# Optimization experiments

Hardware: AMD Instinct MI355X
Metric: run time of the kernel (lower is better)

The kernel has to match this reference:

```python
import jax, jax.numpy as jnp
import numpy as np

N_EMBD = 768
NUM_HEADS = 12
NEG_INF = -1e38


def setup_inputs() -> dict:
    key = jax.random.key(0)
    kx, kq, kk, kv, ko, kb = jax.random.split(key, 6)
    B, S, E = 2, 2048, N_EMBD
    scale = 1.0 / np.sqrt(E)
    return {
        "x": jax.random.normal(kx, (B, S, E), dtype=jnp.float32),
        "Wq": jax.random.normal(kq, (E, E), dtype=jnp.float32) * scale,
        "Wk": jax.random.normal(kk, (E, E), dtype=jnp.float32) * scale,
        "Wv": jax.random.normal(kv, (E, E), dtype=jnp.float32) * scale,
        "Wo": jax.random.normal(ko, (E, E), dtype=jnp.float32) * scale,
        "bo": jax.random.normal(kb, (E,), dtype=jnp.float32) * 0.01,
    }


def reference(x, Wq, Wk, Wv, Wo, bo):
    B, S, E = x.shape
    H = NUM_HEADS
    D = E // H

    def split_heads(t):  # [B,S,E] -> [B,H,S,D]
        return t.reshape(B, S, H, D).transpose(0, 2, 1, 3)

    # torch Linear (no bias): y = x @ W.T
    q = split_heads(jnp.einsum('bse,fe->bsf', x, Wq))
    k = split_heads(jnp.einsum('bse,fe->bsf', x, Wk))
    v = split_heads(jnp.einsum('bse,fe->bsf', x, Wv))

    # NOTE: original module does NOT scale by 1/sqrt(head_dim) — faithful.
    scores = jnp.einsum('bhqd,bhkd->bhqk', q, k)  # [B,H,S,S]
    causal_mask = (1.0 - jnp.tril(jnp.ones((S, S), dtype=x.dtype))) * NEG_INF
    probs = jax.nn.softmax(scores + causal_mask, axis=-1)
    attn = jnp.einsum('bhqk,bhkd->bhqd', probs, v)  # [B,H,S,D]

    merged = attn.transpose(0, 2, 1, 3).reshape(B, S, E)
    out = jnp.einsum('bse,fe->bsf', merged, Wo) + bo
    return (out, k, v)
```

## Files before the change

### kernel.cpp

```cpp
#include <hip/hip_runtime.h>
#include <hip/hip_bf16.h>

#define S_LEN 2048
#define EMB 768
#define NH 12
#define HD 64
#define L2E 1.44269504088896340736f

typedef __attribute__((ext_vector_type(8))) short short8;
typedef __attribute__((ext_vector_type(4))) float f32x4;

typedef __attribute__((address_space(3))) void lds_t;
typedef __attribute__((address_space(1))) const void gbl_t;

__device__ __forceinline__ void gload16(const void* g, void* l) {
  __builtin_amdgcn_global_load_lds((gbl_t*)g, (lds_t*)l, 16, 0, 0);
}

__device__ __forceinline__ short f2bf(float f) {
  union { float f; unsigned u; } v; v.f = f;
  unsigned r = v.u + 0x7FFFu + ((v.u >> 16) & 1u);
  return (short)(r >> 16);
}

__device__ __forceinline__ unsigned pkbf(float a, float b) {
  unsigned r;
  asm("v_cvt_pk_bf16_f32 %0, %1, %2" : "=v"(r) : "v"(a), "v"(b));
  return r;
}

__global__ void cvt_all(const float* __restrict__ x,
                        const float* __restrict__ Wq, const float* __restrict__ Wk,
                        const float* __restrict__ Wv, const float* __restrict__ Wo,
                        short* __restrict__ xb, short* __restrict__ Wb,
                        short* __restrict__ Wob) {
  int bid = blockIdx.x, tid = threadIdx.x;
  const float* src;
  short* dst;
  int off;
  if (bid < 3072) {
    src = x; dst = xb; off = bid * 1024 + tid * 4;
  } else {
    int wb = bid - 3072;
    int sec = wb / 576;
    off = (wb % 576) * 1024 + tid * 4;
    src = sec == 0 ? Wq : sec == 1 ? Wk : sec == 2 ? Wv : Wo;
    dst = sec < 3 ? Wb + sec * 589824 : Wob;
  }
  float4 v = *reinterpret_cast<const float4*>(src + off);
  short4 o;
  o.x = f2bf(v.x); o.y = f2bf(v.y); o.z = f2bf(v.z); o.w = f2bf(v.w);
  *reinterpret_cast<short4*>(dst + off) = o;
}

template<int MODE>
__global__ __launch_bounds__(256)
void gemm_nt(const short* __restrict__ A, const short* __restrict__ B,
             float* __restrict__ outk, float* __restrict__ outv,
             short* __restrict__ qb, short* __restrict__ kb, short* __restrict__ vtb,
             float* __restrict__ outp, const float* __restrict__ bias) {
  const int K = EMB;
  const int NT = K / 64;
  __shared__ __align__(16) char RAW[128 * 132 * 4];
  short (*As)[128][64] = (short(*)[128][64])RAW;
  short (*Bs)[128][64] = (short(*)[128][64])(RAW + 32768);
  float (*Cl)[132] = (float(*)[132])RAW;
  int tid = threadIdx.x;
  int lane = tid & 63, wid = tid >> 6;
  int wm = wid >> 1, wn = wid & 1;
  int r16 = lane & 15, g4 = lane >> 4;
  int m0 = blockIdx.y * 128, n0 = blockIdx.x * 128;
  int lrow = lane >> 3, lchunk = lane & 7;
  int lcolsw = ((lchunk ^ lrow) * 8);
  f32x4 acc[4][4] = {};

#define STAGEG(BUF, K0) do {                                          \
    _Pragma("unroll")                                                 \
    for (int i = 0; i < 4; i++) {                                     \
      int r = wid * 32 + i * 8 + lrow;                                \
      gload16(A + (long)(m0 + r) * K + (K0) + lcolsw, &As[BUF][r][lchunk * 8]); \
      gload16(B + (long)(n0 + r) * K + (K0) + lcolsw, &Bs[BUF][r][lchunk * 8]); \
    } } while (0)

  STAGEG(0, 0);
  int cur = 0;
  for (int t = 0; t < NT; t++) {
    if (t + 1 < NT) {
      STAGEG(cur ^ 1, (t + 1) * 64);
      asm volatile("s_waitcnt vmcnt(8)" ::: "memory");
    } else {
      asm volatile("s_waitcnt vmcnt(0)" ::: "memory");
    }
    __builtin_amdgcn_sched_barrier(0);
    __builtin_amdgcn_s_barrier();
    __builtin_amdgcn_sched_barrier(0);
#pragma unroll
    for (int s = 0; s < 2; s++) {
      int csw = ((s * 4 + g4) ^ (r16 & 7)) * 8;
      short8 af[4], bf[4];
#pragma unroll
      for (int tt = 0; tt < 4; tt++) {
        af[tt] = *reinterpret_cast<const short8*>(&As[cur][wm * 64 + tt * 16 + r16][csw]);
        bf[tt] = *reinterpret_cast<const short8*>(&Bs[cur][wn * 64 + tt * 16 + r16][csw]);
      }
#pragma unroll
      for (int mt = 0; mt < 4; mt++)
#pragma unroll
        for (int nt = 0; nt < 4; nt++)
          acc[mt][nt] = __builtin_amdgcn_mfma_f32_16x16x32_bf16(af[mt], bf[nt], acc[mt][nt], 0, 0, 0);
    }
    __builtin_amdgcn_sched_barrier(0);
    __builtin_amdgcn_s_barrier();
    cur ^= 1;
  }
#undef STAGEG

  if (MODE == 1) {
#pragma unroll
    for (int mt = 0; mt < 4; mt++) {
      int nbase = m0 + wm * 64 + mt * 16 + g4 * 4;
#pragma unroll
      for (int nt = 0; nt < 4; nt++) {
        int f = n0 + wn * 64 + nt * 16 + r16;
#pragma unroll
        for (int r = 0; r < 4; r++)
          outp[(long)(nbase + r) * EMB + f] = acc[mt][nt][r] + bias[f];
      }
    }
    return;
  }

  const int bx = blockIdx.x;
  const int sec = bx / 6;
  const int h0 = (bx % 6) * 2;
  const int b = m0 >> 11, s0l = m0 & 2047;

  if (sec == 2) {
#pragma unroll
    for (int mt = 0; mt < 4; mt++) {
      int sg = s0l + wm * 64 + mt * 16 + g4 * 4;
#pragma unroll
      for (int nt = 0; nt < 4; nt++) {
        int fl = wn * 64 + nt * 16 + r16;
        int h = h0 + (fl >> 6), d = fl & 63;
        int bh = b * NH + h;
        short4 o;
        o.x = f2bf(acc[mt][nt][0]); o.y = f2bf(acc[mt][nt][1]);
        o.z = f2bf(acc[mt][nt][2]); o.w = f2bf(acc[mt][nt][3]);
        *reinterpret_cast<short4*>(
            &vtb[((long)(bh * 32 + (sg >> 6)) * 64 + d) * 64 + (sg & 63)]) = o;
      }
    }
  }

#pragma unroll
  for (int mt = 0; mt < 4; mt++) {
    int rl = wm * 64 + mt * 16 + g4 * 4;
#pragma unroll
    for (int nt = 0; nt < 4; nt++) {
      int fl = wn * 64 + nt * 16 + r16;
#pragma unroll
      for (int r = 0; r < 4; r++) Cl[rl + r][fl] = acc[mt][nt][r];
    }
  }
  __syncthreads();

  {
    int row = tid >> 1, cb = (tid & 1) * 32;
#pragma unroll
    for (int hh = 0; hh < 2; hh++) {
      const float* src = &Cl[row][hh * 64 + cb];
      long base = ((long)(b * NH + h0 + hh) * S_LEN + s0l) * HD + (long)row * 64 + cb;
      if (sec == 0) {
        short* dq = qb + base;
#pragma unroll
        for (int c = 0; c < 4; c++) {
          f32x4 a = *reinterpret_cast<const f32x4*>(src + c * 8);
          f32x4 bb = *reinterpret_cast<const f32x4*>(src + c * 8 + 4);
          short8 o;
#pragma unroll
          for (int j = 0; j < 4; j++) { o[j] = f2bf(a[j]); o[4 + j] = f2bf(bb[j]); }
          *reinterpret_cast<short8*>(dq + c * 8) = o;
        }
      } else if (sec == 1) {
        float* dk = outk + base;
        short* dkb = kb + base;
#pragma unroll
        for (int c = 0; c < 4; c++) {
          f32x4 a = *reinterpret_cast<const f32x4*>(src + c * 8);
          f32x4 bb = *reinterpret_cast<const f32x4*>(src + c * 8 + 4);
          *reinterpret_cast<f32x4*>(dk + c * 8) = a;
          *reinterpret_cast<f32x4*>(dk + c * 8 + 4) = bb;
          short8 o;
#pragma unroll
          for (int j = 0; j < 4; j++) { o[j] = f2bf(a[j]); o[4 + j] = f2bf(bb[j]); }
          *reinterpret_cast<short8*>(dkb + c * 8) = o;
        }
      } else {
        float* dv = outv + base;
#pragma unroll
        for (int c = 0; c < 8; c++)
          *reinterpret_cast<f32x4*>(dv + c * 4) =
              *reinterpret_cast<const f32x4*>(src + c * 4);
      }
    }
  }
}

__global__ __launch_bounds__(256)
void flash_attn15(const short* __restrict__ qb, const short* __restrict__ kb,
                  const short* __restrict__ vtb, short* __restrict__ mb) {
  const int tid = threadIdx.x;
  const int w = tid >> 6, lane = tid & 63;
  const int r16 = lane & 15, g4 = lane >> 4;
  const int id = blockIdx.x;
  const int xcd = id & 7, u = id >> 3;
  const int bh = xcd + 8 * (u % 3);
  const int qt = 31 - u / 3;
  const int q0 = qt * 64 + w * 16;
  const int nkt = qt + 1;

  const short* qh = qb + (long)bh * S_LEN * HD;
  const short* kh = kb + (long)bh * S_LEN * HD;
  const short* vh = vtb + (long)bh * S_LEN * HD;

  __shared__ __align__(16) short KVl[2][2][64][64];
  __shared__ __align__(16) short Pa[4][16][40];
  __shared__ __align__(16) short Pb[4][16][40];
  __shared__ __align__(16) float sca_lds[4][16];
  float* Olds = (float*)&KVl[0][0][0][0];

  const int srow = tid >> 3, schunk = tid & 7;
  const short* ksrc = kh + srow * HD + ((schunk ^ (srow & 7)) * 8);
  const short* vsrc = vh + srow * 64 + ((schunk ^ (srow & 7)) * 8);
#define STAGE(BUF, KT) do {                                          \
    long _off = (long)(KT) * 4096;                                   \
    gload16(ksrc + _off,           &KVl[BUF][0][srow][schunk * 8]);      \
    gload16(ksrc + _off + 32 * HD, &KVl[BUF][0][srow + 32][schunk * 8]); \
    gload16(vsrc + _off,           &KVl[BUF][1][srow][schunk * 8]);      \
    gload16(vsrc + _off + 32 * 64, &KVl[BUF][1][srow + 32][schunk * 8]); \
  } while (0)

  short8 qf0 = *reinterpret_cast<const short8*>(qh + (q0 + r16) * HD + g4 * 8);
  short8 qf1 = *reinterpret_cast<const short8*>(qh + (q0 + r16) * HD + 32 + g4 * 8);

  float m0 = -1e30f, m20 = -1.44e30f;
  float l0 = 0.f;
  f32x4 oacc[4] = {};

  const int kc0 = (g4 ^ (r16 & 7)) * 8;

  STAGE(0, 0);

  for (int kt = 0; kt < nkt; kt++) {
    __syncthreads();
    if (kt + 1 < nkt) STAGE((kt + 1) & 1, kt + 1);

    const short* kbuf = &KVl[kt & 1][0][0][0];
    const short* vbuf = &KVl[kt & 1][1][0][0];

    short8 k00 = *reinterpret_cast<const short8*>(kbuf + (r16) * 64 + kc0);
    short8 k01 = *reinterpret_cast<const short8*>(kbuf + (r16) * 64 + (kc0 ^ 32));
    short8 k10 = *reinterpret_cast<const short8*>(kbuf + (16 + r16) * 64 + kc0);
    short8 k11 = *reinterpret_cast<const short8*>(kbuf + (16 + r16) * 64 + (kc0 ^ 32));
    short8 k20 = *reinterpret_cast<const short8*>(kbuf + (32 + r16) * 64 + kc0);
    short8 k21 = *reinterpret_cast<const short8*>(kbuf + (32 + r16) * 64 + (kc0 ^ 32));
    short8 k30 = *reinterpret_cast<const short8*>(kbuf + (48 + r16) * 64 + kc0);
    short8 k31 = *reinterpret_cast<const short8*>(kbuf + (48 + r16) * 64 + (kc0 ^ 32));

    f32x4 s0 = {0.f, 0.f, 0.f, 0.f}, s1 = {0.f, 0.f, 0.f, 0.f};
    f32x4 s2 = {0.f, 0.f, 0.f, 0.f}, s3 = {0.f, 0.f, 0.f, 0.f};
    s0 = __builtin_amdgcn_mfma_f32_16x16x32_bf16(k00, qf0, s0, 0, 0, 0);
    s0 = __builtin_amdgcn_mfma_f32_16x16x32_bf16(k01, qf1, s0, 0, 0, 0);
    s1 = __builtin_amdgcn_mfma_f32_16x16x32_bf16(k10, qf0, s1, 0, 0, 0);
    s1 = __builtin_amdgcn_mfma_f32_16x16x32_bf16(k11, qf1, s1, 0, 0, 0);
    s2 = __builtin_amdgcn_mfma_f32_16x16x32_bf16(k20, qf0, s2, 0, 0, 0);
    s2 = __builtin_amdgcn_mfma_f32_16x16x32_bf16(k21, qf1, s2, 0, 0, 0);
    s3 = __builtin_amdgcn_mfma_f32_16x16x32_bf16(k30, qf0, s3, 0, 0, 0);
    s3 = __builtin_amdgcn_mfma_f32_16x16x32_bf16(k31, qf1, s3, 0, 0, 0);

    if (kt == nkt - 1) {
      int qg = q0 + r16;
#pragma unroll
      for (int r = 0; r < 4; r++) {
        int kbase = kt * 64 + g4 * 4 + r;
        if (kbase > qg)      s0[r] = -1e30f;
        if (kbase + 16 > qg) s1[r] = -1e30f;
        if (kbase + 32 > qg) s2[r] = -1e30f;
        if (kbase + 48 > qg) s3[r] = -1e30f;
      }
    }

    float rm_local = fmaxf(
        fmaxf(fmaxf(fmaxf(s0[0], s0[1]), fmaxf(s0[2], s0[3])),
              fmaxf(fmaxf(s1[0], s1[1]), fmaxf(s1[2], s1[3]))),
        fmaxf(fmaxf(fmaxf(s2[0], s2[1]), fmaxf(s2[2], s2[3])),
              fmaxf(fmaxf(s3[0], s3[1]), fmaxf(s3[2], s3[3]))));

    if (!__all(rm_local <= m0 + 8.f)) {
      float x = rm_local;
      x = fmaxf(x, __shfl_xor(x, 16));
      x = fmaxf(x, __shfl_xor(x, 32));
      float nm = fmaxf(m0, x);
      float sca = __builtin_exp2f((m0 - nm) * L2E);
      m0 = nm; m20 = nm * L2E; l0 *= sca;
      if (g4 == 0) sca_lds[w][r16] = sca;
      f32x4 sr = *reinterpret_cast<const f32x4*>(&sca_lds[w][g4 * 4]);
#pragma unroll
      for (int dt = 0; dt < 4; dt++)
#pragma unroll
        for (int r = 0; r < 4; r++) oacc[dt][r] *= sr[r];
    }

    float rs = 0.f;
#pragma unroll
    for (int r = 0; r < 4; r++) {
      s0[r] = __builtin_exp2f(fmaf(s0[r], L2E, -m20));
      s1[r] = __builtin_exp2f(fmaf(s1[r], L2E, -m20));
      s2[r] = __builtin_exp2f(fmaf(s2[r], L2E, -m20));
      s3[r] = __builtin_exp2f(fmaf(s3[r], L2E, -m20));
      rs += (s0[r] + s1[r]) + (s2[r] + s3[r]);
    }
    l0 += rs;

    {
      uint2 wv;
      wv.x = pkbf(s0[0], s0[1]); wv.y = pkbf(s0[2], s0[3]);
      *reinterpret_cast<uint2*>(&Pa[w][r16][g4 * 4]) = wv;
      wv.x = pkbf(s1[0], s1[1]); wv.y = pkbf(s1[2], s1[3]);
      *reinterpret_cast<uint2*>(&Pa[w][r16][16 + g4 * 4]) = wv;
      wv.x = pkbf(s2[0], s2[1]); wv.y = pkbf(s2[2], s2[3]);
      *reinterpret_cast<uint2*>(&Pb[w][r16][g4 * 4]) = wv;
      wv.x = pkbf(s3[0], s3[1]); wv.y = pkbf(s3[2], s3[3]);
      *reinterpret_cast<uint2*>(&Pb[w][r16][16 + g4 * 4]) = wv;
    }
    short8 pa0 = *reinterpret_cast<const short8*>(&Pa[w][r16][g4 * 8]);
    short8 pa1 = *reinterpret_cast<const short8*>(&Pb[w][r16][g4 * 8]);

    short8 v00 = *reinterpret_cast<const short8*>(vbuf + (r16) * 64 + kc0);
    short8 v01 = *reinterpret_cast<const short8*>(vbuf + (r16) * 64 + (kc0 ^ 32));
    short8 v10 = *reinterpret_cast<const short8*>(vbuf + (16 + r16) * 64 + kc0);
    short8 v11 = *reinterpret_cast<const short8*>(vbuf + (16 + r16) * 64 + (kc0 ^ 32));
    short8 v20 = *reinterpret_cast<const short8*>(vbuf + (32 + r16) * 64 + kc0);
    short8 v21 = *reinterpret_cast<const short8*>(vbuf + (32 + r16) * 64 + (kc0 ^ 32));
    short8 v30 = *reinterpret_cast<const short8*>(vbuf + (48 + r16) * 64 + kc0);
    short8 v31 = *reinterpret_cast<const short8*>(vbuf + (48 + r16) * 64 + (kc0 ^ 32));

    oacc[0] = __builtin_amdgcn_mfma_f32_16x16x32_bf16(pa0, v00, oacc[0], 0, 0, 0);
    oacc[0] = __builtin_amdgcn_mfma_f32_16x16x32_bf16(pa1, v01, oacc[0], 0, 0, 0);
    oacc[1] = __builtin_amdgcn_mfma_f32_16x16x32_bf16(pa0, v10, oacc[1], 0, 0, 0);
    oacc[1] = __builtin_amdgcn_mfma_f32_16x16x32_bf16(pa1, v11, oacc[1], 0, 0, 0);
    oacc[2] = __builtin_amdgcn_mfma_f32_16x16x32_bf16(pa0, v20, oacc[2], 0, 0, 0);
    oacc[2] = __builtin_amdgcn_mfma_f32_16x16x32_bf16(pa1, v21, oacc[2], 0, 0, 0);
    oacc[3] = __builtin_amdgcn_mfma_f32_16x16x32_bf16(pa0, v30, oacc[3], 0, 0, 0);
    oacc[3] = __builtin_amdgcn_mfma_f32_16x16x32_bf16(pa1, v31, oacc[3], 0, 0, 0);
  }
#undef STAGE

  __syncthreads();

  {
    float rs = l0;
    rs += __shfl_xor(rs, 16);
    rs += __shfl_xor(rs, 32);
    if (g4 == 0) sca_lds[w][r16] = rs;
  }
  f32x4 li = *reinterpret_cast<const f32x4*>(&sca_lds[w][g4 * 4]);
  f32x4 iv;
#pragma unroll
  for (int r = 0; r < 4; r++) iv[r] = 1.f / li[r];
  float* Ow = Olds + w * 16 * 68;
#pragma unroll
  for (int dt = 0; dt < 4; dt++)
#pragma unroll
    for (int r = 0; r < 4; r++)
      Ow[(g4 * 4 + r) * 68 + dt * 16 + r16] = oacc[dt][r] * iv[r];
  {
    int orow = lane >> 2, oc = (lane & 3) * 16;
    int bb = bh / NH, h = bh % NH;
    f32x4 a0 = *reinterpret_cast<const f32x4*>(&Ow[orow * 68 + oc]);
    f32x4 a1 = *reinterpret_cast<const f32x4*>(&Ow[orow * 68 + oc + 4]);
    f32x4 a2 = *reinterpret_cast<const f32x4*>(&Ow[orow * 68 + oc + 8]);
    f32x4 a3 = *reinterpret_cast<const f32x4*>(&Ow[orow * 68 + oc + 12]);
    short8 sa, sb;
#pragma unroll
    for (int j = 0; j < 4; j++) {
      sa[j] = f2bf(a0[j]); sa[4 + j] = f2bf(a1[j]);
      sb[j] = f2bf(a2[j]); sb[4 + j] = f2bf(a3[j]);
    }
    short* dst = &mb[((long)(bb * S_LEN + q0 + orow)) * EMB + h * HD + oc];
    *reinterpret_cast<short8*>(dst) = sa;
    *reinterpret_cast<short8*>(dst + 8) = sb;
  }
}

extern "C" void kernel_launch(void* const* d_in, const int* in_sizes, int n_in,
                              void* d_out, int out_size, void* d_ws, size_t ws_size,
                              hipStream_t stream) {
  const float* x  = (const float*)d_in[0];
  const float* Wq = (const float*)d_in[1];
  const float* Wk = (const float*)d_in[2];
  const float* Wv = (const float*)d_in[3];
  const float* Wo = (const float*)d_in[4];
  const float* bo = (const float*)d_in[5];

  float* out  = (float*)d_out;
  float* outk = out + 3145728;
  float* outv = out + 6291456;

  short* ws  = (short*)d_ws;
  short* xb  = ws;
  short* Wb  = xb + 3145728;
  short* Wob = Wb + 1769472;
  short* qb  = Wob + 589824;
  short* kb  = qb + 3145728;
  short* vtb = kb + 3145728;
  short* mb  = vtb + 3145728;

  cvt_all<<<5376, 256, 0, stream>>>(x, Wq, Wk, Wv, Wo, xb, Wb, Wob);

  gemm_nt<0><<<dim3(18, 32), 256, 0, stream>>>(xb, Wb, outk, outv, qb, kb, vtb, nullptr, nullptr);
  flash_attn15<<<768, 256, 0, stream>>>(qb, kb, vtb, mb);
  gemm_nt<1><<<dim3(6, 32), 256, 0, stream>>>(mb, Wob, nullptr, nullptr, nullptr, nullptr, nullptr, out, bo);
}
```

Measured before the change: 103.4 us.

## Give each attention wave two query row tiles and halve block size

The flash-attention kernel now runs 2 waves per block instead of 4, and each wave handles 32 query rows (two 16-row tiles) rather than 16. Each K/V fragment read from LDS is reused across both query tiles, which halves LDS traffic per MFMA, and the staging loop is restructured for 128 threads. The cost is more accumulator and score registers per wave and fewer waves per block to hide latency, which may lower occupancy or overlap.

```diff
diff --git a/kernel.cpp b/kernel.cpp
--- a/kernel.cpp
+++ b/kernel.cpp
@@ -207,8 +207,8 @@
   }
 }
 
-__global__ __launch_bounds__(256)
-void flash_attn15(const short* __restrict__ qb, const short* __restrict__ kb,
+__global__ __launch_bounds__(128)
+void flash_attn16(const short* __restrict__ qb, const short* __restrict__ kb,
                   const short* __restrict__ vtb, short* __restrict__ mb) {
   const int tid = threadIdx.x;
   const int w = tid >> 6, lane = tid & 63;
@@ -217,36 +217,41 @@
   const int xcd = id & 7, u = id >> 3;
   const int bh = xcd + 8 * (u % 3);
   const int qt = 31 - u / 3;
-  const int q0 = qt * 64 + w * 16;
+  const int q0 = qt * 64 + w * 32;
   const int nkt = qt + 1;
 
   const short* qh = qb + (long)bh * S_LEN * HD;
   const short* kh = kb + (long)bh * S_LEN * HD;
   const short* vh = vtb + (long)bh * S_LEN * HD;
 
-  __shared__ __align__(16) short KVl[2][2][64][64];
-  __shared__ __align__(16) short Pa[4][16][40];
-  __shared__ __align__(16) short Pb[4][16][40];
-  __shared__ __align__(16) float sca_lds[4][16];
-  float* Olds = (float*)&KVl[0][0][0][0];
+  __shared__ __align__(16) char RAW[42240];
+  short (*KVl)[2][64][64] = (short(*)[2][64][64])RAW;
+  short (*Pa)[32][36] = (short(*)[32][36])(RAW + 32768);
+  short (*Pb)[32][36] = (short(*)[32][36])(RAW + 32768 + 4608);
+  float (*sca_lds)[32] = (float(*)[32])(RAW + 41984);
 
   const int srow = tid >> 3, schunk = tid & 7;
   const short* ksrc = kh + srow * HD + ((schunk ^ (srow & 7)) * 8);
   const short* vsrc = vh + srow * 64 + ((schunk ^ (srow & 7)) * 8);
-#define STAGE(BUF, KT) do {                                          \
-    long _off = (long)(KT) * 4096;                                   \
-    gload16(ksrc + _off,           &KVl[BUF][0][srow][schunk * 8]);      \
-    gload16(ksrc + _off + 32 * HD, &KVl[BUF][0][srow + 32][schunk * 8]); \
-    gload16(vsrc + _off,           &KVl[BUF][1][srow][schunk * 8]);      \
-    gload16(vsrc + _off + 32 * 64, &KVl[BUF][1][srow + 32][schunk * 8]); \
-  } while (0)
-
-  short8 qf0 = *reinterpret_cast<const short8*>(qh + (q0 + r16) * HD + g4 * 8);
-  short8 qf1 = *reinterpret_cast<const short8*>(qh + (q0 + r16) * HD + 32 + g4 * 8);
-
-  float m0 = -1e30f, m20 = -1.44e30f;
-  float l0 = 0.f;
-  f32x4 oacc[4] = {};
+#define STAGE(BUF, KT) do {                                              \
+    long _off = (long)(KT) * 4096;                                       \
+    _Pragma("unroll")                                                    \
+    for (int j = 0; j < 4; j++) {                                        \
+      gload16(ksrc + _off + j * 16 * HD, &KVl[BUF][0][srow + 16 * j][schunk * 8]); \
+      gload16(vsrc + _off + j * 16 * 64, &KVl[BUF][1][srow + 16 * j][schunk * 8]); \
+    } } while (0)
+
+  short8 qf[2][2];
+#pragma unroll
+  for (int ct = 0; ct < 2; ct++)
+#pragma unroll
+    for (int ksl = 0; ksl < 2; ksl++)
+      qf[ct][ksl] = *reinterpret_cast<const short8*>(
+          qh + (q0 + ct * 16 + r16) * HD + ksl * 32 + g4 * 8);
+
+  float m[2] = {-1e30f, -1e30f}, m2[2] = {-1.44e30f, -1.44e30f};
+  float l[2] = {0.f, 0.f};
+  f32x4 oacc[2][4] = {};
 
   const int kc0 = (g4 ^ (r16 & 7)) * 8;
 
@@ -259,138 +264,144 @@
     const short* kbuf = &KVl[kt & 1][0][0][0];
     const short* vbuf = &KVl[kt & 1][1][0][0];
 
-    short8 k00 = *reinterpret_cast<const short8*>(kbuf + (r16) * 64 + kc0);
-    short8 k01 = *reinterpret_cast<const short8*>(kbuf + (r16) * 64 + (kc0 ^ 32));
-    short8 k10 = *reinterpret_cast<const short8*>(kbuf + (16 + r16) * 64 + kc0);
-    short8 k11 = *reinterpret_cast<const short8*>(kbuf + (16 + r16) * 64 + (kc0 ^ 32));
-    short8 k20 = *reinterpret_cast<const short8*>(kbuf + (32 + r16) * 64 + kc0);
-    short8 k21 = *reinterpret_cast<const short8*>(kbuf + (32 + r16) * 64 + (kc0 ^ 32));
-    short8 k30 = *reinterpret_cast<const short8*>(kbuf + (48 + r16) * 64 + kc0);
-    short8 k31 = *reinterpret_cast<const short8*>(kbuf + (48 + r16) * 64 + (kc0 ^ 32));
-
-    f32x4 s0 = {0.f, 0.f, 0.f, 0.f}, s1 = {0.f, 0.f, 0.f, 0.f};
-    f32x4 s2 = {0.f, 0.f, 0.f, 0.f}, s3 = {0.f, 0.f, 0.f, 0.f};
-    s0 = __builtin_amdgcn_mfma_f32_16x16x32_bf16(k00, qf0, s0, 0, 0, 0);
-    s0 = __builtin_amdgcn_mfma_f32_16x16x32_bf16(k01, qf1, s0, 0, 0, 0);
-    s1 = __builtin_amdgcn_mfma_f32_16x16x32_bf16(k10, qf0, s1, 0, 0, 0);
-    s1 = __builtin_amdgcn_mfma_f32_16x16x32_bf16(k11, qf1, s1, 0, 0, 0);
-    s2 = __builtin_amdgcn_mfma_f32_16x16x32_bf16(k20, qf0, s2, 0, 0, 0);
-    s2 = __builtin_amdgcn_mfma_f32_16x16x32_bf16(k21, qf1, s2, 0, 0, 0);
-    s3 = __builtin_amdgcn_mfma_f32_16x16x32_bf16(k30, qf0, s3, 0, 0, 0);
-    s3 = __builtin_amdgcn_mfma_f32_16x16x32_bf16(k31, qf1, s3, 0, 0, 0);
+    f32x4 s[4][2] = {};
+#pragma unroll
+    for (int kb = 0; kb < 4; kb++) {
+      short8 k0 = *reinterpret_cast<const short8*>(kbuf + (kb * 16 + r16) * 64 + kc0);
+      short8 k1 = *reinterpret_cast<const short8*>(kbuf + (kb * 16 + r16) * 64 + (kc0 ^ 32));
+#pragma unroll
+      for (int ct = 0; ct < 2; ct++) {
+        s[kb][ct] = __builtin_amdgcn_mfma_f32_16x16x32_bf16(k0, qf[ct][0], s[kb][ct], 0, 0, 0);
+        s[kb][ct] = __builtin_amdgcn_mfma_f32_16x16x32_bf16(k1, qf[ct][1], s[kb][ct], 0, 0, 0);
+      }
+    }
 
     if (kt == nkt - 1) {
-      int qg = q0 + r16;
-#pragma unroll
-      for (int r = 0; r < 4; r++) {
-        int kbase = kt * 64 + g4 * 4 + r;
-        if (kbase > qg)      s0[r] = -1e30f;
-        if (kbase + 16 > qg) s1[r] = -1e30f;
-        if (kbase + 32 > qg) s2[r] = -1e30f;
-        if (kbase + 48 > qg) s3[r] = -1e30f;
-      }
-    }
-
-    float rm_local = fmaxf(
-        fmaxf(fmaxf(fmaxf(s0[0], s0[1]), fmaxf(s0[2], s0[3])),
-              fmaxf(fmaxf(s1[0], s1[1]), fmaxf(s1[2], s1[3]))),
-        fmaxf(fmaxf(fmaxf(s2[0], s2[1]), fmaxf(s2[2], s2[3])),
-              fmaxf(fmaxf(s3[0], s3[1]), fmaxf(s3[2], s3[3]))));
-
-    if (!__all(rm_local <= m0 + 8.f)) {
-      float x = rm_local;
-      x = fmaxf(x, __shfl_xor(x, 16));
-      x = fmaxf(x, __shfl_xor(x, 32));
-      float nm = fmaxf(m0, x);
-      float sca = __builtin_exp2f((m0 - nm) * L2E);
-      m0 = nm; m20 = nm * L2E; l0 *= sca;
-      if (g4 == 0) sca_lds[w][r16] = sca;
-      f32x4 sr = *reinterpret_cast<const f32x4*>(&sca_lds[w][g4 * 4]);
+#pragma unroll
+      for (int ct = 0; ct < 2; ct++) {
+        int qg = q0 + ct * 16 + r16;
+#pragma unroll
+        for (int kb = 0; kb < 4; kb++)
+#pragma unroll
+          for (int r = 0; r < 4; r++)
+            if (kt * 64 + kb * 16 + g4 * 4 + r > qg) s[kb][ct][r] = -1e30f;
+      }
+    }
+
+    float rm[2];
+#pragma unroll
+    for (int ct = 0; ct < 2; ct++) {
+      float a = fmaxf(fmaxf(s[0][ct][0], s[0][ct][1]), fmaxf(s[0][ct][2], s[0][ct][3]));
+      float b = fmaxf(fmaxf(s[1][ct][0], s[1][ct][1]), fmaxf(s[1][ct][2], s[1][ct][3]));
+      float c = fmaxf(fmaxf(s[2][ct][0], s[2][ct][1]), fmaxf(s[2][ct][2], s[2][ct][3]));
+      float d = fmaxf(fmaxf(s[3][ct][0], s[3][ct][1]), fmaxf(s[3][ct][2], s[3][ct][3]));
+      rm[ct] = fmaxf(fmaxf(a, b), fmaxf(c, d));
+    }
+
+    bool cond = (rm[0] <= m[0] + 8.f) && (rm[1] <= m[1] + 8.f);
+    if (!__all(cond)) {
+      float sca[2];
+#pragma unroll
+      for (int ct = 0; ct < 2; ct++) {
+        float x = rm[ct];
+        x = fmaxf(x, __shfl_xor(x, 16));
+        x = fmaxf(x, __shfl_xor(x, 32));
+        float nm = fmaxf(m[ct], x);
+        sca[ct] = __builtin_exp2f((m[ct] - nm) * L2E);
+        m[ct] = nm; m2[ct] = nm * L2E; l[ct] *= sca[ct];
+      }
+      if (g4 == 0) { sca_lds[w][r16] = sca[0]; sca_lds[w][16 + r16] = sca[1]; }
+      f32x4 sr0 = *reinterpret_cast<const f32x4*>(&sca_lds[w][g4 * 4]);
+      f32x4 sr1 = *reinterpret_cast<const f32x4*>(&sca_lds[w][16 + g4 * 4]);
 #pragma unroll
       for (int dt = 0; dt < 4; dt++)
 #pragma unroll
-        for (int r = 0; r < 4; r++) oacc[dt][r] *= sr[r];
-    }
-
-    float rs = 0.f;
+        for (int r = 0; r < 4; r++) {
+          oacc[0][dt][r] *= sr0[r];
+          oacc[1][dt][r] *= sr1[r];
+        }
+    }
+
+    float rs[2] = {0.f, 0.f};
+#pragma unroll
+    for (int kb = 0; kb < 4; kb++)
+#pragma unroll
+      for (int ct = 0; ct < 2; ct++)
+#pragma unroll
+        for (int r = 0; r < 4; r++) {
+          s[kb][ct][r] = __builtin_exp2f(fmaf(s[kb][ct][r], L2E, -m2[ct]));
+          rs[ct] += s[kb][ct][r];
+        }
+    l[0] += rs[0]; l[1] += rs[1];
+
+#pragma unroll
+    for (int kb = 0; kb < 4; kb++)
+#pragma unroll
+      for (int ct = 0; ct < 2; ct++) {
+        uint2 wv;
+        wv.x = pkbf(s[kb][ct][0], s[kb][ct][1]);
+        wv.y = pkbf(s[kb][ct][2], s[kb][ct][3]);
+        short* dstp = (kb < 2) ? &Pa[w][ct * 16 + r16][(kb & 1) * 16 + g4 * 4]
+                               : &Pb[w][ct * 16 + r16][(kb & 1) * 16 + g4 * 4];
+        *reinterpret_cast<uint2*>(dstp) = wv;
+      }
+    short8 pa[2][2];
+#pragma unroll
+    for (int ct = 0; ct < 2; ct++) {
+      pa[ct][0] = *reinterpret_cast<const short8*>(&Pa[w][ct * 16 + r16][g4 * 8]);
+      pa[ct][1] = *reinterpret_cast<const short8*>(&Pb[w][ct * 16 + r16][g4 * 8]);
+    }
+
+#pragma unroll
+    for (int dt = 0; dt < 4; dt++) {
+      short8 v0 = *reinterpret_cast<const short8*>(vbuf + (dt * 16 + r16) * 64 + kc0);
+      short8 v1 = *reinterpret_cast<const short8*>(vbuf + (dt * 16 + r16) * 64 + (kc0 ^ 32));
+#pragma unroll
+      for (int ct = 0; ct < 2; ct++) {
+        oacc[ct][dt] = __builtin_amdgcn_mfma_f32_16x16x32_bf16(pa[ct][0], v0, oacc[ct][dt], 0, 0, 0);
+        oacc[ct][dt] = __builtin_amdgcn_mfma_f32_16x16x32_bf16(pa[ct][1], v1, oacc[ct][dt], 0, 0, 0);
+      }
+    }
+  }
+#undef STAGE
+
+  __syncthreads();
+
+#pragma unroll
+  for (int ct = 0; ct < 2; ct++) {
+    float rsv = l[ct];
+    rsv += __shfl_xor(rsv, 16);
+    rsv += __shfl_xor(rsv, 32);
+    if (g4 == 0) sca_lds[w][ct * 16 + r16] = rsv;
+  }
+  f32x4 li0 = *reinterpret_cast<const f32x4*>(&sca_lds[w][g4 * 4]);
+  f32x4 li1 = *reinterpret_cast<const f32x4*>(&sca_lds[w][16 + g4 * 4]);
+  f32x4 iv0, iv1;
+#pragma unroll
+  for (int r = 0; r < 4; r++) { iv0[r] = 1.f / li0[r]; iv1[r] = 1.f / li1[r]; }
+
+  float* Ow = (float*)(RAW + w * 32 * 68 * 4);
+#pragma unroll
+  for (int dt = 0; dt < 4; dt++)
 #pragma unroll
     for (int r = 0; r < 4; r++) {
-      s0[r] = __builtin_exp2f(fmaf(s0[r], L2E, -m20));
-      s1[r] = __builtin_exp2f(fmaf(s1[r], L2E, -m20));
-      s2[r] = __builtin_exp2f(fmaf(s2[r], L2E, -m20));
-      s3[r] = __builtin_exp2f(fmaf(s3[r], L2E, -m20));
-      rs += (s0[r] + s1[r]) + (s2[r] + s3[r]);
-    }
-    l0 += rs;
-
-    {
-      uint2 wv;
-      wv.x = pkbf(s0[0], s0[1]); wv.y = pkbf(s0[2], s0[3]);
-      *reinterpret_cast<uint2*>(&Pa[w][r16][g4 * 4]) = wv;
-      wv.x = pkbf(s1[0], s1[1]); wv.y = pkbf(s1[2], s1[3]);
-      *reinterpret_cast<uint2*>(&Pa[w][r16][16 + g4 * 4]) = wv;
-      wv.x = pkbf(s2[0], s2[1]); wv.y = pkbf(s2[2], s2[3]);
-      *reinterpret_cast<uint2*>(&Pb[w][r16][g4 * 4]) = wv;
-      wv.x = pkbf(s3[0], s3[1]); wv.y = pkbf(s3[2], s3[3]);
-      *reinterpret_cast<uint2*>(&Pb[w][r16][16 + g4 * 4]) = wv;
-    }
-    short8 pa0 = *reinterpret_cast<const short8*>(&Pa[w][r16][g4 * 8]);
-    short8 pa1 = *reinterpret_cast<const short8*>(&Pb[w][r16][g4 * 8]);
-
-    short8 v00 = *reinterpret_cast<const short8*>(vbuf + (r16) * 64 + kc0);
-    short8 v01 = *reinterpret_cast<const short8*>(vbuf + (r16) * 64 + (kc0 ^ 32));
-    short8 v10 = *reinterpret_cast<const short8*>(vbuf + (16 + r16) * 64 + kc0);
-    short8 v11 = *reinterpret_cast<const short8*>(vbuf + (16 + r16) * 64 + (kc0 ^ 32));
-    short8 v20 = *reinterpret_cast<const short8*>(vbuf + (32 + r16) * 64 + kc0);
-    short8 v21 = *reinterpret_cast<const short8*>(vbuf + (32 + r16) * 64 + (kc0 ^ 32));
-    short8 v30 = *reinterpret_cast<const short8*>(vbuf + (48 + r16) * 64 + kc0);
-    short8 v31 = *reinterpret_cast<const short8*>(vbuf + (48 + r16) * 64 + (kc0 ^ 32));
-
-    oacc[0] = __builtin_amdgcn_mfma_f32_16x16x32_bf16(pa0, v00, oacc[0], 0, 0, 0);
-    oacc[0] = __builtin_amdgcn_mfma_f32_16x16x32_bf16(pa1, v01, oacc[0], 0, 0, 0);
-    oacc[1] = __builtin_amdgcn_mfma_f32_16x16x32_bf16(pa0, v10, oacc[1], 0, 0, 0);
-    oacc[1] = __builtin_amdgcn_mfma_f32_16x16x32_bf16(pa1, v11, oacc[1], 0, 0, 0);
-    oacc[2] = __builtin_amdgcn_mfma_f32_16x16x32_bf16(pa0, v20, oacc[2], 0, 0, 0);
-    oacc[2] = __builtin_amdgcn_mfma_f32_16x16x32_bf16(pa1, v21, oacc[2], 0, 0, 0);
-    oacc[3] = __builtin_amdgcn_mfma_f32_16x16x32_bf16(pa0, v30, oacc[3], 0, 0, 0);
-    oacc[3] = __builtin_amdgcn_mfma_f32_16x16x32_bf16(pa1, v31, oacc[3], 0, 0, 0);
-  }
-#undef STAGE
-
-  __syncthreads();
-
+      Ow[(g4 * 4 + r) * 68 + dt * 16 + r16] = oacc[0][dt][r] * iv0[r];
+      Ow[(16 + g4 * 4 + r) * 68 + dt * 16 + r16] = oacc[1][dt][r] * iv1[r];
+    }
   {
-    float rs = l0;
-    rs += __shfl_xor(rs, 16);
-    rs += __shfl_xor(rs, 32);
-    if (g4 == 0) sca_lds[w][r16] = rs;
-  }
-  f32x4 li = *reinterpret_cast<const f32x4*>(&sca_lds[w][g4 * 4]);
-  f32x4 iv;
-#pragma unroll
-  for (int r = 0; r < 4; r++) iv[r] = 1.f / li[r];
-  float* Ow = Olds + w * 16 * 68;
-#pragma unroll
-  for (int dt = 0; dt < 4; dt++)
-#pragma unroll
-    for (int r = 0; r < 4; r++)
-      Ow[(g4 * 4 + r) * 68 + dt * 16 + r16] = oacc[dt][r] * iv[r];
-  {
-    int orow = lane >> 2, oc = (lane & 3) * 16;
+    int row = lane >> 1, cb = (lane & 1) * 32;
     int bb = bh / NH, h = bh % NH;
-    f32x4 a0 = *reinterpret_cast<const f32x4*>(&Ow[orow * 68 + oc]);
-    f32x4 a1 = *reinterpret_cast<const f32x4*>(&Ow[orow * 68 + oc + 4]);
-    f32x4 a2 = *reinterpret_cast<const f32x4*>(&Ow[orow * 68 + oc + 8]);
-    f32x4 a3 = *reinterpret_cast<const f32x4*>(&Ow[orow * 68 + oc + 12]);
-    short8 sa, sb;
-#pragma unroll
-    for (int j = 0; j < 4; j++) {
-      sa[j] = f2bf(a0[j]); sa[4 + j] = f2bf(a1[j]);
-      sb[j] = f2bf(a2[j]); sb[4 + j] = f2bf(a3[j]);
-    }
-    short* dst = &mb[((long)(bb * S_LEN + q0 + orow)) * EMB + h * HD + oc];
-    *reinterpret_cast<short8*>(dst) = sa;
-    *reinterpret_cast<short8*>(dst + 8) = sb;
+    const float* src = &Ow[row * 68 + cb];
+    short* dst = &mb[((long)(bb * S_LEN + q0 + row)) * EMB + h * HD + cb];
+#pragma unroll
+    for (int c = 0; c < 4; c++) {
+      f32x4 a = *reinterpret_cast<const f32x4*>(src + c * 8);
+      f32x4 b2 = *reinterpret_cast<const f32x4*>(src + c * 8 + 4);
+      short8 o;
+#pragma unroll
+      for (int j = 0; j < 4; j++) { o[j] = f2bf(a[j]); o[4 + j] = f2bf(b2[j]); }
+      *reinterpret_cast<short8*>(dst + c * 8) = o;
+    }
   }
 }
 
@@ -420,6 +431,6 @@
   cvt_all<<<5376, 256, 0, stream>>>(x, Wq, Wk, Wv, Wo, xb, Wb, Wob);
 
   gemm_nt<0><<<dim3(18, 32), 256, 0, stream>>>(xb, Wb, outk, outv, qb, kb, vtb, nullptr, nullptr);
-  flash_attn15<<<768, 256, 0, stream>>>(qb, kb, vtb, mb);
+  flash_attn16<<<768, 128, 0, stream>>>(qb, kb, vtb, mb);
   gemm_nt<1><<<dim3(6, 32), 256, 0, stream>>>(mb, Wob, nullptr, nullptr, nullptr, nullptr, nullptr, out, bo);
 }
```

After: 123.5 us. 1.19x slower.
